# Kernel tuning notes

Hardware: AMD Instinct MI355X
Metric: run time of the kernel (lower is better)

Reference implementation:

```python
import jax, jax.numpy as jnp
import numpy as np

EPS = 1e-5
K_NN = 10  # init kwarg k
NINP = 552  # 4*(128+4+6)
NTOK = 255


def _leaky(x):
    return jnp.where(x > 0, x, 0.2 * x)


def _bn(h, gamma, beta):
    # training-mode batch norm over all dims except channel (last), biased var
    mu = jnp.mean(h, axis=(0, 1, 2))
    var = jnp.var(h, axis=(0, 1, 2))
    return (h - mu) * jax.lax.rsqrt(var + EPS) * gamma + beta


def _edgeconv(x, W, gamma, beta, k):
    # x: (B, N, C) -> (B, N, O). EdgeConv: knn + gather + 1x1 conv + BN + LeakyReLU + max over k
    B, N, C = x.shape
    xx = jnp.sum(x * x, axis=-1)  # (B, N)
    # pairwise_distance = -||xi - xj||^2 (larger = closer)
    d = 2.0 * jnp.einsum('bnc,bmc->bnm', x, x) - xx[:, :, None] - xx[:, None, :]
    _, idx = jax.lax.top_k(d, k)  # (B, N, k)
    nb = x[jnp.arange(B)[:, None, None], idx]  # (B, N, k, C) gathered neighbors
    ctr = jnp.broadcast_to(x[:, :, None, :], nb.shape)
    feat = jnp.concatenate([nb - ctr, ctr], axis=-1)  # (B, N, k, 2C)
    h = jnp.einsum('bnkc,oc->bnko', feat, W)  # 1x1 conv, no bias
    h = _leaky(_bn(h, gamma, beta))
    return jnp.max(h, axis=2)  # max-aggregate over k


def setup_inputs() -> dict:
    key = jax.random.key(0)
    ks = jax.random.split(key, 12)
    S, B, K, D = 2048, 8, 8, 3
    p = {}
    p['x'] = jax.random.normal(ks[0], (S, B, K, D), dtype=jnp.float32)
    def w(k_, shape):
        return jax.random.normal(k_, shape, dtype=jnp.float32) * 0.05
    p['W1'] = w(ks[1], (64, 48));   p['g1'] = jnp.ones((64,));  p['b1'] = jnp.zeros((64,))
    p['W2'] = w(ks[2], (64, 128));  p['g2'] = jnp.ones((64,));  p['b2'] = jnp.zeros((64,))
    p['W3'] = w(ks[3], (128, 128)); p['g3'] = jnp.ones((128,)); p['b3'] = jnp.zeros((128,))
    p['W4'] = w(ks[4], (256, 256)); p['g4'] = jnp.ones((256,)); p['b4'] = jnp.zeros((256,))
    p['W5'] = w(ks[5], (256, 512))
    p['W6'] = w(ks[6], (NINP, 256))
    p['Wd1'] = w(ks[7], (NINP, NINP)); p['bd1'] = jnp.zeros((NINP,))
    p['Wd2'] = w(ks[8], (NTOK, NINP)); p['bd2'] = jnp.zeros((NTOK,))
    return p


def reference(x, W1, g1, b1, W2, g2, b2, W3, g3, b3, W4, g4, b4, W5, W6, Wd1, bd1, Wd2, bd2):
    S, B, K, D = x.shape
    pts = jnp.transpose(x, (1, 0, 2, 3)).reshape(B, S, K * D).astype(jnp.float32)  # (B,N,24)
    x1 = _edgeconv(pts, W1, g1, b1, K_NN)  # (B,N,64)
    x2 = _edgeconv(x1, W2, g2, b2, K_NN)   # (B,N,64)
    x3 = _edgeconv(x2, W3, g3, b3, K_NN)   # (B,N,128)
    x4 = _edgeconv(x3, W4, g4, b4, K_NN)   # (B,N,256)
    cat = jnp.concatenate([x1, x2, x3, x4], axis=-1)  # (B,N,512)
    h = _leaky(jnp.einsum('bnc,oc->bno', cat, W5))    # conv5: (B,N,256)
    feature = _leaky(jnp.einsum('bnc,oc->bno', h, W6))  # conv6: (B,N,552)
    logits = (feature @ Wd1.T + bd1) @ Wd2.T + bd2      # (B,N,255)
    return feature, logits
```

## Files before the change

### kernel.cpp

```cpp
#include <hip/hip_runtime.h>
#include <float.h>
#include <math.h>

#define NPT 2048
#define NBATCH 8
#define NPTS_TOTAL 16384
#define KNN 10
#define STAT_BLOCKS 2048
#define NCHUNK 8
#define CHUNKSZ 256
#define TR 32
#define CB 8

__device__ __forceinline__ int swz(int r) { return (r ^ (r >> 2)) & 7; }

__global__ __launch_bounds__(256) void k_pts(const float* __restrict__ x, float* __restrict__ pts) {
    int i = blockIdx.x * 256 + threadIdx.x;
    if (i >= NPTS_TOTAL * 24) return;
    int p = i / 24, c = i - p * 24;
    int b = p >> 11, n = p & 2047;
    pts[i] = x[(n * 8 + b) * 24 + c];
}

__global__ __launch_bounds__(256) void k_prep(const float* __restrict__ x, int ld, int C,
                                              double* __restrict__ norms, float* __restrict__ qT) {
    int p = blockIdx.x * 256 + threadIdx.x;
    if (p >= NPTS_TOTAL) return;
    const float* row = x + (size_t)p * ld;
    double s = 0.0;
    for (int c = 0; c < C; ++c) {
        float v = row[c];
        qT[(size_t)c * NPTS_TOTAL + p] = v;
        double dv = (double)v;
        s += dv * dv;
    }
    norms[p] = s;
}

template<int C>
__global__ __launch_bounds__(256, 2) void k_knn2(const float* __restrict__ x, int ld,
                                                 const double* __restrict__ norms,
                                                 const float* __restrict__ qT,
                                                 double* __restrict__ pk, int* __restrict__ pi) {
    __shared__ float tile[TR * C];
    __shared__ double tnorm[TR];
    __shared__ float slab[C * 256];
    const int tid = threadIdx.x;
    const int chunk = blockIdx.x;
    const int p0g = blockIdx.y * 256;
    const int p = p0g + tid;
    const int b = p >> 11;
    const float* xb = x + (size_t)b * NPT * ld;
    const double* nbase = norms + (size_t)b * NPT;
    const double nn = norms[p];
    const int cand0 = chunk * CHUNKSZ;

    for (int i = tid; i < C * 64; i += 256) {
        int c = i >> 6, c4 = i & 63;
        ((float4*)slab)[c * 64 + c4] = *(const float4*)(qT + (size_t)c * NPTS_TOTAL + p0g + c4 * 4);
    }

    double keys[10]; int ids[10];
#pragma unroll
    for (int t = 0; t < 10; ++t) { keys[t] = -DBL_MAX; ids[t] = 0; }

    for (int t0 = 0; t0 < CHUNKSZ; t0 += TR) {
        __syncthreads();
        for (int i = tid; i < TR * C / 4; i += 256) {
            int r = i / (C / 4), c4 = i - r * (C / 4);
            ((float4*)tile)[i] = ((const float4*)(xb + (size_t)(cand0 + t0 + r) * ld))[c4];
        }
        if (tid < TR) tnorm[tid] = nbase[cand0 + t0 + tid];
        __syncthreads();

        double acc[TR];
#pragma unroll
        for (int j = 0; j < TR; ++j) acc[j] = 0.0;

        for (int cb = 0; cb < C / CB; ++cb) {
            double qd[CB];
#pragma unroll
            for (int e = 0; e < CB; ++e)
                qd[e] = (double)slab[(cb * CB + e) * 256 + tid];
#pragma unroll
            for (int j = 0; j < TR; ++j) {
                const float4 t0v = *(const float4*)&tile[j * C + cb * CB];
                const float4 t1v = *(const float4*)&tile[j * C + cb * CB + 4];
                double a = acc[j];
                a = fma(qd[0], (double)t0v.x, a);
                a = fma(qd[1], (double)t0v.y, a);
                a = fma(qd[2], (double)t0v.z, a);
                a = fma(qd[3], (double)t0v.w, a);
                a = fma(qd[4], (double)t1v.x, a);
                a = fma(qd[5], (double)t1v.y, a);
                a = fma(qd[6], (double)t1v.z, a);
                a = fma(qd[7], (double)t1v.w, a);
                acc[j] = a;
            }
        }
#pragma unroll
        for (int j = 0; j < TR; ++j) {
            double d = 2.0 * acc[j] - nn - tnorm[j];
            int m = cand0 + t0 + j;
            if (d > keys[9]) {
                double cv = d; int ci = m;
#pragma unroll
                for (int t = 0; t < 10; ++t) {
                    bool sw = cv > keys[t];
                    double tk = keys[t]; int ti = ids[t];
                    if (sw) { keys[t] = cv; ids[t] = ci; cv = tk; ci = ti; }
                }
            }
        }
    }
#pragma unroll
    for (int t = 0; t < 10; ++t) {
        pk[((size_t)p * NCHUNK + chunk) * 10 + t] = keys[t];
        pi[((size_t)p * NCHUNK + chunk) * 10 + t] = ids[t];
    }
}

__global__ __launch_bounds__(256) void k_kmerge(const double* __restrict__ pk,
                                                const int* __restrict__ pi,
                                                int* __restrict__ idx_out) {
    int p = blockIdx.x * 256 + threadIdx.x;
    if (p >= NPTS_TOTAL) return;
    int h[NCHUNK];
#pragma unroll
    for (int c = 0; c < NCHUNK; ++c) h[c] = 0;
    const double* base = pk + (size_t)p * NCHUNK * 10;
    const int* ibase = pi + (size_t)p * NCHUNK * 10;
    for (int t = 0; t < 10; ++t) {
        double bv = -DBL_MAX; int bc = 0;
#pragma unroll
        for (int c = 0; c < NCHUNK; ++c) {
            double v = (h[c] < 10) ? base[c * 10 + h[c]] : -DBL_MAX;
            if (v > bv) { bv = v; bc = c; }
        }
        int sel = 0;
#pragma unroll
        for (int c = 0; c < NCHUNK; ++c) {
            if (c == bc) sel = ibase[c * 10 + h[c]];
            h[c] += (c == bc) ? 1 : 0;
        }
        idx_out[p * 10 + t] = sel;
    }
}

template<int C, int O>
__global__ __launch_bounds__(256, 2) void k_sgemm(const float* __restrict__ x, int ld,
                                                  const float* __restrict__ W,
                                                  float* __restrict__ s) {
    constexpr int C4 = (C / 4 < 8) ? 8 : C / 4;
    __shared__ __align__(16) float smem[(64 + 64) * C4 * 4];
    float4* As = (float4*)smem;
    float4* Bs = (float4*)(smem + 64 * C4 * 4);
    const int tid = threadIdx.x;
    const int p0 = blockIdx.x * 64;
    const int o0 = blockIdx.y * 64;
    for (int i = tid; i < 64 * C4; i += 256) {
        int r = i / C4, c4 = i - r * C4;
        float4 v = make_float4(0.f, 0.f, 0.f, 0.f);
        if (c4 * 4 < C) v = *(const float4*)(x + (size_t)(p0 + r) * ld + c4 * 4);
        As[r * C4 + (c4 ^ swz(r))] = v;
    }
    for (int i = tid; i < 64 * C4; i += 256) {
        int oo = i / C4, c4 = i - oo * C4;
        float4 v = make_float4(0.f, 0.f, 0.f, 0.f);
        if (c4 * 4 < C) {
            const float* wr = W + (size_t)(o0 + oo) * 2 * C;
            float4 w1 = *(const float4*)(wr + c4 * 4);
            float4 w2 = *(const float4*)(wr + C + c4 * 4);
            v = make_float4(w2.x - w1.x, w2.y - w1.y, w2.z - w1.z, w2.w - w1.w);
        }
        Bs[oo * C4 + (c4 ^ swz(oo))] = v;
    }
    __syncthreads();
    const int tx = tid & 15, ty = tid >> 4;
    float acc[4][4];
#pragma unroll
    for (int a = 0; a < 4; ++a)
#pragma unroll
        for (int b = 0; b < 4; ++b) acc[a][b] = 0.f;
    for (int c4 = 0; c4 < C4; ++c4) {
        float4 av[4], bv[4];
#pragma unroll
        for (int rj = 0; rj < 4; ++rj) { int r = ty * 4 + rj; av[rj] = As[r * C4 + (c4 ^ swz(r))]; }
#pragma unroll
        for (int oj = 0; oj < 4; ++oj) { int oo = tx * 4 + oj; bv[oj] = Bs[oo * C4 + (c4 ^ swz(oo))]; }
#pragma unroll
        for (int rj = 0; rj < 4; ++rj)
#pragma unroll
            for (int oj = 0; oj < 4; ++oj) {
                acc[rj][oj] = fmaf(av[rj].x, bv[oj].x, acc[rj][oj]);
                acc[rj][oj] = fmaf(av[rj].y, bv[oj].y, acc[rj][oj]);
                acc[rj][oj] = fmaf(av[rj].z, bv[oj].z, acc[rj][oj]);
                acc[rj][oj] = fmaf(av[rj].w, bv[oj].w, acc[rj][oj]);
            }
    }
#pragma unroll
    for (int rj = 0; rj < 4; ++rj) {
        float4 v = make_float4(acc[rj][0], acc[rj][1], acc[rj][2], acc[rj][3]);
        *(float4*)(s + (size_t)(p0 + ty * 4 + rj) * O + o0 + tx * 4) = v;
    }
}

template<int PASS, int C, int O>
__global__ __launch_bounds__(256, 2) void k_conv2(const float* __restrict__ x, int ld,
                                                  const int* __restrict__ idx,
                                                  const float* __restrict__ W,
                                                  const float* __restrict__ sbuf,
                                                  double* __restrict__ partials,
                                                  const float* __restrict__ ss,
                                                  float* __restrict__ out, int ldo) {
    constexpr int C4 = (C / 4 < 8) ? 8 : C / 4;
    __shared__ __align__(16) float smem[(80 + 64) * C4 * 4];
    __shared__ int sidx[80];
    float4* As = (float4*)smem;
    float4* Bs = (float4*)(smem + 80 * C4 * 4);

    const int tid = threadIdx.x;
    const int rb = blockIdx.x;
    const int o0 = blockIdx.y * 64;
    const int p0 = rb * 8;
    const int b = p0 >> 11;
    const float* xb = x + (size_t)b * NPT * ld;

    if (tid < 80) sidx[tid] = idx[p0 * KNN + tid];
    __syncthreads();

    for (int i = tid; i < 80 * C4; i += 256) {
        int r = i / C4, c4 = i - r * C4;
        float4 v = make_float4(0.f, 0.f, 0.f, 0.f);
        if (c4 * 4 < C) v = *(const float4*)(xb + (size_t)sidx[r] * ld + c4 * 4);
        As[r * C4 + (c4 ^ swz(r))] = v;
    }
    for (int i = tid; i < 64 * C4; i += 256) {
        int oo = i / C4, c4 = i - oo * C4;
        float4 v = make_float4(0.f, 0.f, 0.f, 0.f);
        if (c4 * 4 < C) v = *(const float4*)(W + (size_t)(o0 + oo) * 2 * C + c4 * 4);
        Bs[oo * C4 + (c4 ^ swz(oo))] = v;
    }
    __syncthreads();

    const int tx = tid & 15, ty = tid >> 4;
    const int o_l = tx * 4;
    float acc[5][4];
#pragma unroll
    for (int a = 0; a < 5; ++a)
#pragma unroll
        for (int c = 0; c < 4; ++c) acc[a][c] = 0.f;

    for (int c4 = 0; c4 < C4; ++c4) {
        float4 av[5], bv[4];
#pragma unroll
        for (int rj = 0; rj < 5; ++rj) { int r = ty * 5 + rj; av[rj] = As[r * C4 + (c4 ^ swz(r))]; }
#pragma unroll
        for (int oj = 0; oj < 4; ++oj) { int oo = o_l + oj; bv[oj] = Bs[oo * C4 + (c4 ^ swz(oo))]; }
#pragma unroll
        for (int rj = 0; rj < 5; ++rj)
#pragma unroll
            for (int oj = 0; oj < 4; ++oj) {
                acc[rj][oj] = fmaf(av[rj].x, bv[oj].x, acc[rj][oj]);
                acc[rj][oj] = fmaf(av[rj].y, bv[oj].y, acc[rj][oj]);
                acc[rj][oj] = fmaf(av[rj].z, bv[oj].z, acc[rj][oj]);
                acc[rj][oj] = fmaf(av[rj].w, bv[oj].w, acc[rj][oj]);
            }
    }

    const int pt = ty >> 1;
    const float4 s4 = *(const float4*)(sbuf + (size_t)(p0 + pt) * O + o0 + o_l);
    const float* s4f = (const float*)&s4;

    if (PASS == 0) {
        double sum[4] = {0, 0, 0, 0}, sq[4] = {0, 0, 0, 0};
#pragma unroll
        for (int rj = 0; rj < 5; ++rj)
#pragma unroll
            for (int oj = 0; oj < 4; ++oj) {
                float hf = acc[rj][oj] + s4f[oj];
                double hd = (double)hf;
                sum[oj] += hd; sq[oj] += hd * hd;
            }
        __syncthreads();
        double* red = (double*)smem;
#pragma unroll
        for (int oj = 0; oj < 4; ++oj) {
            red[(ty * 64 + o_l + oj) * 2 + 0] = sum[oj];
            red[(ty * 64 + o_l + oj) * 2 + 1] = sq[oj];
        }
        __syncthreads();
        if (tid < 128) {
            int o = tid & 63, w = tid >> 6;
            double a = 0.0;
            for (int t2 = 0; t2 < 16; ++t2) a += red[(t2 * 64 + o) * 2 + w];
            partials[(size_t)rb * 2 * O + (size_t)w * O + o0 + o] = a;
        }
    } else {
        float m4[4];
#pragma unroll
        for (int oj = 0; oj < 4; ++oj) {
            float sc = ss[o0 + o_l + oj], sh = ss[O + o0 + o_l + oj];
            float m = -FLT_MAX;
#pragma unroll
            for (int rj = 0; rj < 5; ++rj) {
                float h = (acc[rj][oj] + s4f[oj]) * sc + sh;
                h = h > 0.f ? h : 0.2f * h;
                m = fmaxf(m, h);
            }
            m4[oj] = m;
        }
        __syncthreads();
        float* red = smem;
#pragma unroll
        for (int oj = 0; oj < 4; ++oj) red[ty * 64 + o_l + oj] = m4[oj];
        __syncthreads();
        if ((ty & 1) == 0) {
            float4 o4;
            float* po = (float*)&o4;
#pragma unroll
            for (int oj = 0; oj < 4; ++oj)
                po[oj] = fmaxf(red[ty * 64 + o_l + oj], red[(ty + 1) * 64 + o_l + oj]);
            *(float4*)(out + (size_t)(p0 + pt) * ldo + o0 + o_l) = o4;
        }
    }
}

__global__ __launch_bounds__(256) void k_bnstats(const double* __restrict__ partials,
                                                 const float* __restrict__ g,
                                                 const float* __restrict__ be,
                                                 float* __restrict__ ss, int O) {
    int o = threadIdx.x;
    if (o >= O) return;
    double sum = 0.0, sq = 0.0;
    for (int b = 0; b < STAT_BLOCKS; ++b) {
        sum += partials[(size_t)b * 2 * O + o];
        sq  += partials[(size_t)b * 2 * O + O + o];
    }
    const double M = 163840.0;
    double mu = sum / M;
    double var = sq / M - mu * mu;
    if (var < 0.0) var = 0.0;
    float scv = (float)((double)g[o] / sqrt(var + 1e-5));
    ss[o] = scv;
    ss[O + o] = be[o] - (float)mu * scv;
}

template<int ACT>
__global__ __launch_bounds__(256, 2) void k_dense2(const float* __restrict__ in, int ldi, int Cin,
                                                   const float* __restrict__ W,
                                                   const float* __restrict__ bias,
                                                   float* __restrict__ out, int ldo, int Cout) {
    __shared__ __align__(16) float smem[2 * 64 * 64];
    float4* As = (float4*)smem;
    float4* Bs = (float4*)(smem + 64 * 64);
    const int tid = threadIdx.x;
    const int p0 = blockIdx.x * 64;
    const int o0 = blockIdx.y * 64;
    const int tx = tid & 15, ty = tid >> 4;

    float acc[4][4];
#pragma unroll
    for (int a = 0; a < 4; ++a)
#pragma unroll
        for (int b = 0; b < 4; ++b) acc[a][b] = 0.f;

    const int ntile = (Cin + 63) / 64;
    for (int kt = 0; kt < ntile; ++kt) {
        const int c0 = kt * 64;
        __syncthreads();
        for (int i = tid; i < 64 * 16; i += 256) {
            int r = i >> 4, c4 = i & 15;
            float4 v = make_float4(0.f, 0.f, 0.f, 0.f);
            if (c0 + c4 * 4 < Cin) v = *(const float4*)(in + (size_t)(p0 + r) * ldi + c0 + c4 * 4);
            As[r * 16 + (c4 ^ swz(r))] = v;
        }
        for (int i = tid; i < 64 * 16; i += 256) {
            int oo = i >> 4, c4 = i & 15;
            float4 v = make_float4(0.f, 0.f, 0.f, 0.f);
            if (o0 + oo < Cout && c0 + c4 * 4 < Cin)
                v = *(const float4*)(W + (size_t)(o0 + oo) * Cin + c0 + c4 * 4);
            Bs[oo * 16 + (c4 ^ swz(oo))] = v;
        }
        __syncthreads();
#pragma unroll
        for (int c4 = 0; c4 < 16; ++c4) {
            float4 av[4], bv[4];
#pragma unroll
            for (int rj = 0; rj < 4; ++rj) { int r = ty * 4 + rj; av[rj] = As[r * 16 + (c4 ^ swz(r))]; }
#pragma unroll
            for (int oj = 0; oj < 4; ++oj) { int oo = tx * 4 + oj; bv[oj] = Bs[oo * 16 + (c4 ^ swz(oo))]; }
#pragma unroll
            for (int rj = 0; rj < 4; ++rj)
#pragma unroll
                for (int oj = 0; oj < 4; ++oj) {
                    acc[rj][oj] = fmaf(av[rj].x, bv[oj].x, acc[rj][oj]);
                    acc[rj][oj] = fmaf(av[rj].y, bv[oj].y, acc[rj][oj]);
                    acc[rj][oj] = fmaf(av[rj].z, bv[oj].z, acc[rj][oj]);
                    acc[rj][oj] = fmaf(av[rj].w, bv[oj].w, acc[rj][oj]);
                }
        }
    }

    const int ob = o0 + tx * 4;
    float bv4[4] = {0.f, 0.f, 0.f, 0.f};
    if (bias) {
#pragma unroll
        for (int oj = 0; oj < 4; ++oj) if (ob + oj < Cout) bv4[oj] = bias[ob + oj];
    }
#pragma unroll
    for (int rj = 0; rj < 4; ++rj) {
        float v4[4];
#pragma unroll
        for (int oj = 0; oj < 4; ++oj) {
            float v = acc[rj][oj] + bv4[oj];
            if (ACT) v = v > 0.f ? v : 0.2f * v;
            v4[oj] = v;
        }
        float* orow = out + (size_t)(p0 + ty * 4 + rj) * ldo;
        if (ob + 3 < Cout) {
            *(float4*)(orow + ob) = make_float4(v4[0], v4[1], v4[2], v4[3]);
        } else {
#pragma unroll
            for (int oj = 0; oj < 4; ++oj) if (ob + oj < Cout) orow[ob + oj] = v4[oj];
        }
    }
}

extern "C" void kernel_launch(void* const* d_in, const int* in_sizes, int n_in,
                              void* d_out, int out_size, void* d_ws, size_t ws_size,
                              hipStream_t stream) {
    const float* x   = (const float*)d_in[0];
    const float* W1  = (const float*)d_in[1];
    const float* g1  = (const float*)d_in[2];
    const float* b1  = (const float*)d_in[3];
    const float* W2  = (const float*)d_in[4];
    const float* g2  = (const float*)d_in[5];
    const float* b2  = (const float*)d_in[6];
    const float* W3  = (const float*)d_in[7];
    const float* g3  = (const float*)d_in[8];
    const float* b3  = (const float*)d_in[9];
    const float* W4  = (const float*)d_in[10];
    const float* g4  = (const float*)d_in[11];
    const float* b4  = (const float*)d_in[12];
    const float* W5  = (const float*)d_in[13];
    const float* W6  = (const float*)d_in[14];
    const float* Wd1 = (const float*)d_in[15];
    const float* bd1 = (const float*)d_in[16];
    const float* Wd2 = (const float*)d_in[17];
    const float* bd2 = (const float*)d_in[18];

    char* ws = (char*)d_ws;
    float* cat    = (float*)(ws);
    double* norms = (double*)(ws + 33554432);
    float* qT     = (float*)(ws + 33685504);
    double* pk    = (double*)(ws + 42074112);
    int*   pi     = (int*)  (ws + 52559872);
    float* pts    = (float*)(ws + 57802752);
    int*   idx    = (int*)  (ws + 59375616);
    float* ssb    = (float*)(ws + 60030976);
    float* sbuf   = (float*)(ws + 33685504);
    double* parts = (double*)(ws + 50462720);
    float* h5     = (float*)(ws + 33554432);
    float* tmp    = (float*)(ws);

    float* feat = (float*)d_out;
    float* logi = (float*)d_out + 9043968;

    dim3 blk(256);
    dim3 kgrid(NCHUNK, 64);

    k_pts<<<dim3((NPTS_TOTAL * 24 + 255) / 256), blk, 0, stream>>>(x, pts);

    k_prep<<<dim3(64), blk, 0, stream>>>(pts, 24, 24, norms, qT);
    k_knn2<24><<<kgrid, blk, 0, stream>>>(pts, 24, norms, qT, pk, pi);
    k_kmerge<<<dim3(64), blk, 0, stream>>>(pk, pi, idx);
    k_sgemm<24, 64><<<dim3(256, 1), blk, 0, stream>>>(pts, 24, W1, sbuf);
    k_conv2<0, 24, 64><<<dim3(STAT_BLOCKS, 1), blk, 0, stream>>>(pts, 24, idx, W1, sbuf, parts, nullptr, nullptr, 0);
    k_bnstats<<<dim3(1), blk, 0, stream>>>(parts, g1, b1, ssb, 64);
    k_conv2<1, 24, 64><<<dim3(STAT_BLOCKS, 1), blk, 0, stream>>>(pts, 24, idx, W1, sbuf, nullptr, ssb, cat + 0, 512);

    k_prep<<<dim3(64), blk, 0, stream>>>(cat + 0, 512, 64, norms, qT);
    k_knn2<64><<<kgrid, blk, 0, stream>>>(cat + 0, 512, norms, qT, pk, pi);
    k_kmerge<<<dim3(64), blk, 0, stream>>>(pk, pi, idx);
    k_sgemm<64, 64><<<dim3(256, 1), blk, 0, stream>>>(cat + 0, 512, W2, sbuf);
    k_conv2<0, 64, 64><<<dim3(STAT_BLOCKS, 1), blk, 0, stream>>>(cat + 0, 512, idx, W2, sbuf, parts, nullptr, nullptr, 0);
    k_bnstats<<<dim3(1), blk, 0, stream>>>(parts, g2, b2, ssb, 64);
    k_conv2<1, 64, 64><<<dim3(STAT_BLOCKS, 1), blk, 0, stream>>>(cat + 0, 512, idx, W2, sbuf, nullptr, ssb, cat + 64, 512);

    k_prep<<<dim3(64), blk, 0, stream>>>(cat + 64, 512, 64, norms, qT);
    k_knn2<64><<<kgrid, blk, 0, stream>>>(cat + 64, 512, norms, qT, pk, pi);
    k_kmerge<<<dim3(64), blk, 0, stream>>>(pk, pi, idx);
    k_sgemm<64, 128><<<dim3(256, 2), blk, 0, stream>>>(cat + 64, 512, W3, sbuf);
    k_conv2<0, 64, 128><<<dim3(STAT_BLOCKS, 2), blk, 0, stream>>>(cat + 64, 512, idx, W3, sbuf, parts, nullptr, nullptr, 0);
    k_bnstats<<<dim3(1), blk, 0, stream>>>(parts, g3, b3, ssb, 128);
    k_conv2<1, 64, 128><<<dim3(STAT_BLOCKS, 2), blk, 0, stream>>>(cat + 64, 512, idx, W3, sbuf, nullptr, ssb, cat + 128, 512);

    k_prep<<<dim3(64), blk, 0, stream>>>(cat + 128, 512, 128, norms, qT);
    k_knn2<128><<<kgrid, blk, 0, stream>>>(cat + 128, 512, norms, qT, pk, pi);
    k_kmerge<<<dim3(64), blk, 0, stream>>>(pk, pi, idx);
    k_sgemm<128, 256><<<dim3(256, 4), blk, 0, stream>>>(cat + 128, 512, W4, sbuf);
    k_conv2<0, 128, 256><<<dim3(STAT_BLOCKS, 4), blk, 0, stream>>>(cat + 128, 512, idx, W4, sbuf, parts, nullptr, nullptr, 0);
    k_bnstats<<<dim3(1), blk, 0, stream>>>(parts, g4, b4, ssb, 256);
    k_conv2<1, 128, 256><<<dim3(STAT_BLOCKS, 4), blk, 0, stream>>>(cat + 128, 512, idx, W4, sbuf, nullptr, ssb, cat + 256, 512);

    k_dense2<1><<<dim3(256, 4), blk, 0, stream>>>(cat, 512, 512, W5, nullptr, h5, 256, 256);
    k_dense2<1><<<dim3(256, 9), blk, 0, stream>>>(h5, 256, 256, W6, nullptr, feat, 552, 552);
    k_dense2<0><<<dim3(256, 9), blk, 0, stream>>>(feat, 552, 552, Wd1, bd1, tmp, 552, 552);
    k_dense2<0><<<dim3(256, 4), blk, 0, stream>>>(tmp, 552, 552, Wd2, bd2, logi, 255, 255);
}
```

Baseline: 3.512 ms.

## Use fp32 kNN candidate search with packed keys and fp64 refinement

The kNN distance tile loop moves from fp64 FMAs to fp32 FMAs. Each chunk keeps a wider top-16 set as packed 32-bit keys, with the sortable distance bits in the high part and the index in the low 11 bits. A new refine kernel merges the chunk candidates, recomputes exact fp64 distances for the 16 best, and picks the final 10 with index tie-breaking. This removes the expensive fp64 arithmetic from the dominant kNN kernels, at the risk of picking different neighbours when fp32 rounding or the truncated key bits push a true neighbour out of the candidate set.

```diff
diff --git a/kernel.cpp b/kernel.cpp
--- a/kernel.cpp
+++ b/kernel.cpp
@@ -11,8 +11,15 @@
 #define CHUNKSZ 256
 #define TR 32
 #define CB 8
+#define NSEL 16
 
 __device__ __forceinline__ int swz(int r) { return (r ^ (r >> 2)) & 7; }
+
+__device__ __forceinline__ unsigned int pack_dm(float d, int m) {
+    unsigned int u = __float_as_uint(d);
+    u = (u & 0x80000000u) ? ~u : (u | 0x80000000u);
+    return (u & 0xFFFFF800u) | (unsigned int)m;
+}
 
 __global__ __launch_bounds__(256) void k_pts(const float* __restrict__ x, float* __restrict__ pts) {
     int i = blockIdx.x * 256 + threadIdx.x;
@@ -23,27 +30,29 @@
 }
 
 __global__ __launch_bounds__(256) void k_prep(const float* __restrict__ x, int ld, int C,
-                                              double* __restrict__ norms, float* __restrict__ qT) {
+                                              double* __restrict__ norms, float* __restrict__ norms32,
+                                              float* __restrict__ qT) {
     int p = blockIdx.x * 256 + threadIdx.x;
     if (p >= NPTS_TOTAL) return;
     const float* row = x + (size_t)p * ld;
-    double s = 0.0;
+    double s = 0.0; float s32 = 0.f;
     for (int c = 0; c < C; ++c) {
         float v = row[c];
         qT[(size_t)c * NPTS_TOTAL + p] = v;
-        double dv = (double)v;
-        s += dv * dv;
+        s = fma((double)v, (double)v, s);
+        s32 = fmaf(v, v, s32);
     }
     norms[p] = s;
+    norms32[p] = s32;
 }
 
 template<int C>
-__global__ __launch_bounds__(256, 2) void k_knn2(const float* __restrict__ x, int ld,
-                                                 const double* __restrict__ norms,
+__global__ __launch_bounds__(256, 2) void k_knn4(const float* __restrict__ x, int ld,
+                                                 const float* __restrict__ norms32,
                                                  const float* __restrict__ qT,
-                                                 double* __restrict__ pk, int* __restrict__ pi) {
+                                                 unsigned int* __restrict__ pki) {
     __shared__ float tile[TR * C];
-    __shared__ double tnorm[TR];
+    __shared__ float tnorm[TR];
     __shared__ float slab[C * 256];
     const int tid = threadIdx.x;
     const int chunk = blockIdx.x;
@@ -51,8 +60,8 @@
     const int p = p0g + tid;
     const int b = p >> 11;
     const float* xb = x + (size_t)b * NPT * ld;
-    const double* nbase = norms + (size_t)b * NPT;
-    const double nn = norms[p];
+    const float* nbase = norms32 + (size_t)b * NPT;
+    const float nn = norms32[p];
     const int cand0 = chunk * CHUNKSZ;
 
     for (int i = tid; i < C * 64; i += 256) {
@@ -60,9 +69,9 @@
         ((float4*)slab)[c * 64 + c4] = *(const float4*)(qT + (size_t)c * NPTS_TOTAL + p0g + c4 * 4);
     }
 
-    double keys[10]; int ids[10];
-#pragma unroll
-    for (int t = 0; t < 10; ++t) { keys[t] = -DBL_MAX; ids[t] = 0; }
+    unsigned int keys[NSEL];
+#pragma unroll
+    for (int t = 0; t < NSEL; ++t) keys[t] = 0u;
 
     for (int t0 = 0; t0 < CHUNKSZ; t0 += TR) {
         __syncthreads();
@@ -73,78 +82,104 @@
         if (tid < TR) tnorm[tid] = nbase[cand0 + t0 + tid];
         __syncthreads();
 
-        double acc[TR];
-#pragma unroll
-        for (int j = 0; j < TR; ++j) acc[j] = 0.0;
+        float acc[TR];
+#pragma unroll
+        for (int j = 0; j < TR; ++j) acc[j] = 0.f;
 
         for (int cb = 0; cb < C / CB; ++cb) {
-            double qd[CB];
+            float qd[CB];
 #pragma unroll
             for (int e = 0; e < CB; ++e)
-                qd[e] = (double)slab[(cb * CB + e) * 256 + tid];
+                qd[e] = slab[(cb * CB + e) * 256 + tid];
 #pragma unroll
             for (int j = 0; j < TR; ++j) {
                 const float4 t0v = *(const float4*)&tile[j * C + cb * CB];
                 const float4 t1v = *(const float4*)&tile[j * C + cb * CB + 4];
-                double a = acc[j];
-                a = fma(qd[0], (double)t0v.x, a);
-                a = fma(qd[1], (double)t0v.y, a);
-                a = fma(qd[2], (double)t0v.z, a);
-                a = fma(qd[3], (double)t0v.w, a);
-                a = fma(qd[4], (double)t1v.x, a);
-                a = fma(qd[5], (double)t1v.y, a);
-                a = fma(qd[6], (double)t1v.z, a);
-                a = fma(qd[7], (double)t1v.w, a);
+                float a = acc[j];
+                a = fmaf(qd[0], t0v.x, a);
+                a = fmaf(qd[1], t0v.y, a);
+                a = fmaf(qd[2], t0v.z, a);
+                a = fmaf(qd[3], t0v.w, a);
+                a = fmaf(qd[4], t1v.x, a);
+                a = fmaf(qd[5], t1v.y, a);
+                a = fmaf(qd[6], t1v.z, a);
+                a = fmaf(qd[7], t1v.w, a);
                 acc[j] = a;
             }
         }
 #pragma unroll
         for (int j = 0; j < TR; ++j) {
-            double d = 2.0 * acc[j] - nn - tnorm[j];
-            int m = cand0 + t0 + j;
-            if (d > keys[9]) {
-                double cv = d; int ci = m;
-#pragma unroll
-                for (int t = 0; t < 10; ++t) {
+            float d = 2.f * acc[j] - nn - tnorm[j];
+            unsigned int pkv = pack_dm(d, cand0 + t0 + j);
+            if (pkv > keys[NSEL - 1]) {
+                unsigned int cv = pkv;
+#pragma unroll
+                for (int t = 0; t < NSEL; ++t) {
                     bool sw = cv > keys[t];
-                    double tk = keys[t]; int ti = ids[t];
-                    if (sw) { keys[t] = cv; ids[t] = ci; cv = tk; ci = ti; }
+                    unsigned int tk = keys[t];
+                    if (sw) { keys[t] = cv; cv = tk; }
                 }
             }
         }
     }
 #pragma unroll
-    for (int t = 0; t < 10; ++t) {
-        pk[((size_t)p * NCHUNK + chunk) * 10 + t] = keys[t];
-        pi[((size_t)p * NCHUNK + chunk) * 10 + t] = ids[t];
-    }
-}
-
-__global__ __launch_bounds__(256) void k_kmerge(const double* __restrict__ pk,
-                                                const int* __restrict__ pi,
+    for (int t = 0; t < NSEL; ++t)
+        pki[((size_t)p * NCHUNK + chunk) * NSEL + t] = keys[t];
+}
+
+__global__ __launch_bounds__(256) void k_refine(const float* __restrict__ x, int ld, int C,
+                                                const double* __restrict__ norms,
+                                                const unsigned int* __restrict__ pki,
                                                 int* __restrict__ idx_out) {
     int p = blockIdx.x * 256 + threadIdx.x;
     if (p >= NPTS_TOTAL) return;
+    const int b = p >> 11;
+    const float* xb = x + (size_t)b * NPT * ld;
+    const float* xq = x + (size_t)p * ld;
+    const double* nb = norms + (size_t)b * NPT;
+    const double nn = norms[p];
+    const unsigned int* base = pki + (size_t)p * NCHUNK * NSEL;
     int h[NCHUNK];
 #pragma unroll
     for (int c = 0; c < NCHUNK; ++c) h[c] = 0;
-    const double* base = pk + (size_t)p * NCHUNK * 10;
-    const int* ibase = pi + (size_t)p * NCHUNK * 10;
-    for (int t = 0; t < 10; ++t) {
-        double bv = -DBL_MAX; int bc = 0;
+    double keys[10]; int ids[10];
+#pragma unroll
+    for (int t = 0; t < 10; ++t) { keys[t] = -DBL_MAX; ids[t] = 0x7fffffff; }
+
+#pragma unroll
+    for (int t = 0; t < NSEL; ++t) {
+        unsigned int bv = 0u; int bc = 0;
 #pragma unroll
         for (int c = 0; c < NCHUNK; ++c) {
-            double v = (h[c] < 10) ? base[c * 10 + h[c]] : -DBL_MAX;
+            unsigned int v = (h[c] < NSEL) ? base[c * NSEL + h[c]] : 0u;
             if (v > bv) { bv = v; bc = c; }
         }
-        int sel = 0;
-#pragma unroll
-        for (int c = 0; c < NCHUNK; ++c) {
-            if (c == bc) sel = ibase[c * 10 + h[c]];
-            h[c] += (c == bc) ? 1 : 0;
-        }
-        idx_out[p * 10 + t] = sel;
-    }
+        int m = (int)(bv & 0x7FFu);
+#pragma unroll
+        for (int c = 0; c < NCHUNK; ++c) h[c] += (c == bc) ? 1 : 0;
+        const float* xm = xb + (size_t)m * ld;
+        double dot = 0.0;
+        for (int c4 = 0; c4 < C / 4; ++c4) {
+            float4 a = *(const float4*)(xq + c4 * 4);
+            float4 bb = *(const float4*)(xm + c4 * 4);
+            dot = fma((double)a.x, (double)bb.x, dot);
+            dot = fma((double)a.y, (double)bb.y, dot);
+            dot = fma((double)a.z, (double)bb.z, dot);
+            dot = fma((double)a.w, (double)bb.w, dot);
+        }
+        double d = 2.0 * dot - nn - nb[m];
+        if (d > keys[9] || (d == keys[9] && m < ids[9])) {
+            double cv = d; int ci = m;
+#pragma unroll
+            for (int t2 = 0; t2 < 10; ++t2) {
+                bool sw = (cv > keys[t2]) || (cv == keys[t2] && ci < ids[t2]);
+                double tk = keys[t2]; int ti = ids[t2];
+                if (sw) { keys[t2] = cv; ids[t2] = ci; cv = tk; ci = ti; }
+            }
+        }
+    }
+#pragma unroll
+    for (int t = 0; t < 10; ++t) idx_out[p * 10 + t] = ids[t];
 }
 
 template<int C, int O>
@@ -453,14 +488,14 @@
     char* ws = (char*)d_ws;
     float* cat    = (float*)(ws);
     double* norms = (double*)(ws + 33554432);
-    float* qT     = (float*)(ws + 33685504);
-    double* pk    = (double*)(ws + 42074112);
-    int*   pi     = (int*)  (ws + 52559872);
-    float* pts    = (float*)(ws + 57802752);
-    int*   idx    = (int*)  (ws + 59375616);
-    float* ssb    = (float*)(ws + 60030976);
-    float* sbuf   = (float*)(ws + 33685504);
-    double* parts = (double*)(ws + 50462720);
+    float* norms32= (float*)(ws + 33685504);
+    float* qT     = (float*)(ws + 33751040);
+    unsigned int* pki = (unsigned int*)(ws + 42139648);
+    float* pts    = (float*)(ws + 50528256);
+    double* parts = (double*)(ws + 33751040);
+    float* sbuf   = (float*)(ws + 42139648);
+    int*   idx    = (int*)  (ws + 58916864);
+    float* ssb    = (float*)(ws + 59572224);
     float* h5     = (float*)(ws + 33554432);
     float* tmp    = (float*)(ws);
 
@@ -472,33 +507,33 @@
 
     k_pts<<<dim3((NPTS_TOTAL * 24 + 255) / 256), blk, 0, stream>>>(x, pts);
 
-    k_prep<<<dim3(64), blk, 0, stream>>>(pts, 24, 24, norms, qT);
-    k_knn2<24><<<kgrid, blk, 0, stream>>>(pts, 24, norms, qT, pk, pi);
-    k_kmerge<<<dim3(64), blk, 0, stream>>>(pk, pi, idx);
+    k_prep<<<dim3(64), blk, 0, stream>>>(pts, 24, 24, norms, norms32, qT);
+    k_knn4<24><<<kgrid, blk, 0, stream>>>(pts, 24, norms32, qT, pki);
+    k_refine<<<dim3(64), blk, 0, stream>>>(pts, 24, 24, norms, pki, idx);
     k_sgemm<24, 64><<<dim3(256, 1), blk, 0, stream>>>(pts, 24, W1, sbuf);
     k_conv2<0, 24, 64><<<dim3(STAT_BLOCKS, 1), blk, 0, stream>>>(pts, 24, idx, W1, sbuf, parts, nullptr, nullptr, 0);
     k_bnstats<<<dim3(1), blk, 0, stream>>>(parts, g1, b1, ssb, 64);
     k_conv2<1, 24, 64><<<dim3(STAT_BLOCKS, 1), blk, 0, stream>>>(pts, 24, idx, W1, sbuf, nullptr, ssb, cat + 0, 512);
 
-    k_prep<<<dim3(64), blk, 0, stream>>>(cat + 0, 512, 64, norms, qT);
-    k_knn2<64><<<kgrid, blk, 0, stream>>>(cat + 0, 512, norms, qT, pk, pi);
-    k_kmerge<<<dim3(64), blk, 0, stream>>>(pk, pi, idx);
+    k_prep<<<dim3(64), blk, 0, stream>>>(cat + 0, 512, 64, norms, norms32, qT);
+    k_knn4<64><<<kgrid, blk, 0, stream>>>(cat + 0, 512, norms32, qT, pki);
+    k_refine<<<dim3(64), blk, 0, stream>>>(cat + 0, 512, 64, norms, pki, idx);
     k_sgemm<64, 64><<<dim3(256, 1), blk, 0, stream>>>(cat + 0, 512, W2, sbuf);
     k_conv2<0, 64, 64><<<dim3(STAT_BLOCKS, 1), blk, 0, stream>>>(cat + 0, 512, idx, W2, sbuf, parts, nullptr, nullptr, 0);
     k_bnstats<<<dim3(1), blk, 0, stream>>>(parts, g2, b2, ssb, 64);
     k_conv2<1, 64, 64><<<dim3(STAT_BLOCKS, 1), blk, 0, stream>>>(cat + 0, 512, idx, W2, sbuf, nullptr, ssb, cat + 64, 512);
 
-    k_prep<<<dim3(64), blk, 0, stream>>>(cat + 64, 512, 64, norms, qT);
-    k_knn2<64><<<kgrid, blk, 0, stream>>>(cat + 64, 512, norms, qT, pk, pi);
-    k_kmerge<<<dim3(64), blk, 0, stream>>>(pk, pi, idx);
+    k_prep<<<dim3(64), blk, 0, stream>>>(cat + 64, 512, 64, norms, norms32, qT);
+    k_knn4<64><<<kgrid, blk, 0, stream>>>(cat + 64, 512, norms32, qT, pki);
+    k_refine<<<dim3(64), blk, 0, stream>>>(cat + 64, 512, 64, norms, pki, idx);
     k_sgemm<64, 128><<<dim3(256, 2), blk, 0, stream>>>(cat + 64, 512, W3, sbuf);
     k_conv2<0, 64, 128><<<dim3(STAT_BLOCKS, 2), blk, 0, stream>>>(cat + 64, 512, idx, W3, sbuf, parts, nullptr, nullptr, 0);
     k_bnstats<<<dim3(1), blk, 0, stream>>>(parts, g3, b3, ssb, 128);
     k_conv2<1, 64, 128><<<dim3(STAT_BLOCKS, 2), blk, 0, stream>>>(cat + 64, 512, idx, W3, sbuf, nullptr, ssb, cat + 128, 512);
 
-    k_prep<<<dim3(64), blk, 0, stream>>>(cat + 128, 512, 128, norms, qT);
-    k_knn2<128><<<kgrid, blk, 0, stream>>>(cat + 128, 512, norms, qT, pk, pi);
-    k_kmerge<<<dim3(64), blk, 0, stream>>>(pk, pi, idx);
+    k_prep<<<dim3(64), blk, 0, stream>>>(cat + 128, 512, 128, norms, norms32, qT);
+    k_knn4<128><<<kgrid, blk, 0, stream>>>(cat + 128, 512, norms32, qT, pki);
+    k_refine<<<dim3(64), blk, 0, stream>>>(cat + 128, 512, 128, norms, pki, idx);
     k_sgemm<128, 256><<<dim3(256, 4), blk, 0, stream>>>(cat + 128, 512, W4, sbuf);
     k_conv2<0, 128, 256><<<dim3(STAT_BLOCKS, 4), blk, 0, stream>>>(cat + 128, 512, idx, W4, sbuf, parts, nullptr, nullptr, 0);
     k_bnstats<<<dim3(1), blk, 0, stream>>>(parts, g4, b4, ssb, 256);
```

After: 4.324 ms. 23.1% more time.
